# Kernel optimization log

Measured on AMD Instinct MI355X. Metric: run time of the kernel, lower is better.

The kernel has to match this reference:

```python
import jax, jax.numpy as jnp
import numpy as np

TEMP = 0.05
EPS = 1e-8  # matches torch F.cosine_similarity eps default


def setup_inputs() -> dict:
    key = jax.random.key(0)
    k1, k2 = jax.random.split(key)
    B, L, H = 2048, 13, 768
    cls = jax.random.normal(k1, (B, H), dtype=jnp.float32)
    hidden = jax.random.normal(k2, (B, L, H), dtype=jnp.float32)
    return {"cls": cls, "hidden": hidden}


def _normalize(x, axis=-1):
    n = jnp.sqrt(jnp.sum(x * x, axis=axis, keepdims=True))
    return x / jnp.maximum(n, EPS)


def reference(cls, hidden):
    B, L, H = hidden.shape
    cn = _normalize(cls)            # [B, H]
    hn = _normalize(hidden)         # [B, L, H]

    # exp(cos(cls_i, hidden_{i,k}) / temp) -- aligned (diagonal) similarities
    sim_ci_hik = jnp.exp(jnp.einsum('id,ild->il', cn, hn) / TEMP)  # [B, L]

    # exp(cos(cls_i, hidden_{m,n}) / temp) -- all pairs, flattened (m,n)-major
    sim_ci_hmn = jnp.exp(jnp.einsum('id,mnd->imn', cn, hn) / TEMP)  # [B, B, L]
    sim_flat = sim_ci_hmn.reshape(B, B * L)                         # [B, B*L]

    # faithful to original: mask tiles (1 - eye(B)) L times along columns,
    # i.e. zeroes columns c with c % B == i (layout quirk of the source code)
    hmn_mask = jnp.tile(1.0 - jnp.eye(B, dtype=sim_flat.dtype), (1, L))  # [B, B*L]
    s = jnp.sum(sim_flat * hmn_mask, axis=1)                             # [B]

    loss = jnp.mean(-jnp.log(sim_ci_hik) + jnp.log(sim_ci_hik + s[:, None]))
    return loss
```

## Files before the change

### kernel.cpp

```cpp
#include <hip/hip_runtime.h>
#include <cstdint>
#include <cstddef>

#define B_    2048
#define L_    13
#define H_    768
#define NROW  (B_ * L_)
#define RTEMP 20.0f
#define NT    12
#define RS    768
#define NTILE 3328

typedef float f32x4 __attribute__((ext_vector_type(4)));
typedef long  i64x2 __attribute__((ext_vector_type(2)));

static __device__ __forceinline__ unsigned int f2e4m3(float f) {
  unsigned int u = __float_as_uint(f);
  unsigned int s = (u >> 24) & 0x80u;
  unsigned int ua = u & 0x7fffffffu;
  if (ua >= 0x43e80000u) return s | 0x7eu;
  if (ua < 0x3c800000u) {
    int m = (int)rintf(__uint_as_float(ua) * 512.0f);
    return s | (unsigned int)m;
  }
  unsigned int lsb = (ua >> 20) & 1u;
  unsigned int r = ua + 0x7ffffu + lsb;
  int Ee = (int)((r >> 23) & 0xffu) - 127;
  unsigned int mant = (r >> 20) & 7u;
  return s | (unsigned int)(((Ee + 7) << 3) | mant);
}

__device__ __forceinline__ void llds16(const void* g, void* l) {
  __builtin_amdgcn_global_load_lds(
      (const __attribute__((address_space(1))) void*)g,
      (__attribute__((address_space(3))) void*)l, 16, 0, 0);
}

#define BAR do { asm volatile("" ::: "memory");            \
    __builtin_amdgcn_s_barrier();                          \
    asm volatile("" ::: "memory"); } while (0)

#define OFF8(k) ((((k) >> 6) << 6) + (((((k) & 31) >> 3)) << 4) + ((((k) & 32) ? 8 : 0)) + ((k) & 7))

__global__ __launch_bounds__(256) void k_normalize(
    const float* __restrict__ cls, const float* __restrict__ hidden,
    unsigned char* __restrict__ cn8, unsigned char* __restrict__ hn8)
{
  const int wid = threadIdx.x >> 6, lane = threadIdx.x & 63;
  const int row = blockIdx.x * 4 + wid;
  const float4* src; unsigned char* dst;
  if (row < B_) { src = (const float4*)(cls + (size_t)row * H_);           dst = cn8 + (size_t)row * RS; }
  else          { src = (const float4*)(hidden + (size_t)(row - B_) * H_); dst = hn8 + (size_t)(row - B_) * RS; }

  float4 x0 = src[lane], x1 = src[lane + 64], x2 = src[lane + 128];
  float ss = x0.x*x0.x + x0.y*x0.y + x0.z*x0.z + x0.w*x0.w
           + x1.x*x1.x + x1.y*x1.y + x1.z*x1.z + x1.w*x1.w
           + x2.x*x2.x + x2.y*x2.y + x2.z*x2.z + x2.w*x2.w;
#pragma unroll
  for (int m = 1; m < 64; m <<= 1) ss += __shfl_xor(ss, m);
  const float sc = 1.0f / fmaxf(sqrtf(ss), 1e-8f);

  const int k = lane * 4;
  unsigned int p0 = f2e4m3(x0.x*sc) | (f2e4m3(x0.y*sc) << 8) | (f2e4m3(x0.z*sc) << 16) | (f2e4m3(x0.w*sc) << 24);
  unsigned int p1 = f2e4m3(x1.x*sc) | (f2e4m3(x1.y*sc) << 8) | (f2e4m3(x1.z*sc) << 16) | (f2e4m3(x1.w*sc) << 24);
  unsigned int p2 = f2e4m3(x2.x*sc) | (f2e4m3(x2.y*sc) << 8) | (f2e4m3(x2.z*sc) << 16) | (f2e4m3(x2.w*sc) << 24);
  *(unsigned int*)(dst + OFF8(k))       = p0;
  *(unsigned int*)(dst + OFF8(k + 256)) = p1;
  *(unsigned int*)(dst + OFF8(k + 512)) = p2;
}

__global__ __launch_bounds__(256, 4) void k_gemm(
    const unsigned char* __restrict__ cn8,
    const unsigned char* __restrict__ hn8,
    float* __restrict__ S_all,
    float* __restrict__ alignedD)
{
  __shared__ __align__(16) char lds[32768];

  const int tid  = threadIdx.x;
  const int lane = tid & 63;
  const int wid  = tid >> 6;
  const int wm   = wid >> 1;
  const int wn   = wid & 1;
  const int fr   = lane & 15, q = lane >> 4, fr2 = (lane & 15) >> 1;

  const int swz  = ((q | ((fr & 1) << 2)) ^ (fr2 & 7)) << 4;
  const int offA = wm * 4096 + fr2 * 128 + swz;
  const int offB = 8192 + wn * 4096 + fr2 * 128 + swz;

  const int slot_un = (tid & 7) ^ ((tid >> 3) & 7);
  const int srow = 2 * (tid >> 3) + (slot_un >> 2);
  const int scb  = (slot_un & 3) << 4;
  char* ldst = lds + tid * 16;

  const int tile = blockIdx.x;
  const int xcd  = tile & 7;
  const int idx  = tile >> 3;
  const int brow = (idx & 15) << 7;
  const int bcol = (xcd * 26 + (idx >> 4)) << 7;

  const char* gA = (const char*)cn8 + (size_t)(brow + srow) * RS + scb;
  const char* gB = (const char*)hn8 + (size_t)(bcol + srow) * RS + scb;

#define STAGE(sb, t) do {                                         \
    char* d_ = ldst + (sb);                                       \
    const char* a_ = gA + (t) * 64;                               \
    llds16(a_,           d_);                                     \
    llds16(a_ + 64 * RS, d_ + 4096);                              \
    const char* b_ = gB + (t) * 64;                               \
    llds16(b_,           d_ + 8192);                              \
    llds16(b_ + 64 * RS, d_ + 12288);                             \
  } while (0)

  STAGE(0, 0);
  asm volatile("s_waitcnt vmcnt(0)" ::: "memory");
  BAR;

  f32x4 acc[4][4] = {};

  for (int t = 0; t < NT; ++t) {
    if (t + 1 < NT) STAGE(((t + 1) & 1) * 16384, t + 1);

    const char* bb = lds + (t & 1) * 16384;
    i64x2 av[4], bv[4];
#pragma unroll
    for (int i = 0; i < 4; ++i) av[i] = *(const i64x2*)(bb + offA + i * 1024);
#pragma unroll
    for (int i = 0; i < 4; ++i) bv[i] = *(const i64x2*)(bb + offB + i * 1024);

    __builtin_amdgcn_s_setprio(1);
#pragma unroll
    for (int mi = 0; mi < 4; ++mi)
#pragma unroll
      for (int ni = 0; ni < 4; ++ni)
        acc[mi][ni] = __builtin_amdgcn_mfma_f32_16x16x32_fp8_fp8(
            av[mi][0], bv[ni][0], acc[mi][ni], 0, 0, 0);
#pragma unroll
    for (int mi = 0; mi < 4; ++mi)
#pragma unroll
      for (int ni = 0; ni < 4; ++ni)
        acc[mi][ni] = __builtin_amdgcn_mfma_f32_16x16x32_fp8_fp8(
            av[mi][1], bv[ni][1], acc[mi][ni], 0, 0, 0);
    __builtin_amdgcn_s_setprio(0);

    if (t + 1 < NT) {
      asm volatile("s_waitcnt vmcnt(0)" ::: "memory");
      BAR;
    }
  }
#undef STAGE

  const int rowb = brow + wm * 64;
  const int colb = bcol + wn * 64;
#pragma unroll
  for (int mi = 0; mi < 4; ++mi) {
#pragma unroll
    for (int j = 0; j < 4; ++j) {
      const int grow = rowb + mi * 16 + q * 4 + j;
      float v = 0.f;
#pragma unroll
      for (int ni = 0; ni < 4; ++ni) {
        const int gcol = colb + ni * 16 + fr;
        const float a = acc[mi][ni][j];
        if ((unsigned)(gcol - grow * 13) < 13u) alignedD[gcol] = a;
        v += ((gcol & 2047) == grow) ? 0.f : __expf(RTEMP * a);
      }
      v += __shfl_xor(v, 1); v += __shfl_xor(v, 2);
      v += __shfl_xor(v, 4); v += __shfl_xor(v, 8);
      if (fr == 0) atomicAdd(&S_all[grow], v);
    }
  }
}

__global__ __launch_bounds__(256) void k_finalize(
    const float* __restrict__ S_all, const float* __restrict__ alignedD,
    float* __restrict__ out)
{
  const int i = blockIdx.x * 256 + threadIdx.x;
  const int lane = threadIdx.x & 63, wid = threadIdx.x >> 6;
  const float s = S_all[i];
  float accv = 0.f;
#pragma unroll
  for (int l = 0; l < L_; l++) {
    const float d = RTEMP * alignedD[i * L_ + l];
    accv += logf(__expf(d) + s) - d;
  }
#pragma unroll
  for (int m = 1; m < 64; m <<= 1) accv += __shfl_xor(accv, m);
  __shared__ float wsum[4];
  if (lane == 0) wsum[wid] = accv;
  __syncthreads();
  if (threadIdx.x == 0)
    atomicAdd(out, (wsum[0] + wsum[1] + wsum[2] + wsum[3]) * (1.0f / (float)(B_ * L_)));
}

extern "C" void kernel_launch(void* const* d_in, const int* in_sizes, int n_in,
                              void* d_out, int out_size, void* d_ws, size_t ws_size,
                              hipStream_t stream) {
  const float* cls    = (const float*)d_in[0];
  const float* hidden = (const float*)d_in[1];
  float* out = (float*)d_out;

  char* ws = (char*)d_ws;
  unsigned char* hn8 = (unsigned char*)ws;
  unsigned char* cn8 = (unsigned char*)(ws + (size_t)NROW * RS);
  float* S_all    = (float*)(ws + (size_t)NROW * RS + (size_t)B_ * RS);
  float* alignedD = (float*)(ws + (size_t)NROW * RS + (size_t)B_ * RS + B_ * sizeof(float));

  hipMemsetAsync(S_all, 0, B_ * sizeof(float), stream);
  hipMemsetAsync(out, 0, sizeof(float), stream);

  k_normalize<<<(B_ + NROW) / 4, 256, 0, stream>>>(cls, hidden, cn8, hn8);
  k_gemm<<<NTILE, 256, 0, stream>>>(cn8, hn8, S_all, alignedD);
  k_finalize<<<B_ / 256, 256, 0, stream>>>(S_all, alignedD, out);
}
```

Baseline: 101.0 us.

## Give each wave private LDS staging buffers and remove workgroup barriers in GEMM

Each of the four waves now loads its own copy of the A and B sub-tiles it needs into a private 16KB LDS region, double-buffered, and waits only with a per-wave vmcnt counter. This removes the workgroup-wide s_barrier from the main loop. In exchange, LDS use doubles to 64KB and occupancy is lowered to 2 blocks per CU. Global and LDS load traffic also doubles, because each A and B sub-tile is now fetched by two waves. There is a possible hazard: the buffer being refilled may still be read by in-flight LDS reads from the previous iteration, since there is no lgkmcnt wait.

```diff
diff --git a/kernel.cpp b/kernel.cpp
--- a/kernel.cpp
+++ b/kernel.cpp
@@ -35,10 +35,6 @@
       (const __attribute__((address_space(1))) void*)g,
       (__attribute__((address_space(3))) void*)l, 16, 0, 0);
 }
-
-#define BAR do { asm volatile("" ::: "memory");            \
-    __builtin_amdgcn_s_barrier();                          \
-    asm volatile("" ::: "memory"); } while (0)
 
 #define OFF8(k) ((((k) >> 6) << 6) + (((((k) & 31) >> 3)) << 4) + ((((k) & 32) ? 8 : 0)) + ((k) & 7))
 
@@ -69,13 +65,13 @@
   *(unsigned int*)(dst + OFF8(k + 512)) = p2;
 }
 
-__global__ __launch_bounds__(256, 4) void k_gemm(
+__global__ __launch_bounds__(256, 2) void k_gemm(
     const unsigned char* __restrict__ cn8,
     const unsigned char* __restrict__ hn8,
     float* __restrict__ S_all,
     float* __restrict__ alignedD)
 {
-  __shared__ __align__(16) char lds[32768];
+  __shared__ __align__(16) char lds[65536];
 
   const int tid  = threadIdx.x;
   const int lane = tid & 63;
@@ -84,44 +80,52 @@
   const int wn   = wid & 1;
   const int fr   = lane & 15, q = lane >> 4, fr2 = (lane & 15) >> 1;
 
-  const int swz  = ((q | ((fr & 1) << 2)) ^ (fr2 & 7)) << 4;
-  const int offA = wm * 4096 + fr2 * 128 + swz;
-  const int offB = 8192 + wn * 4096 + fr2 * 128 + swz;
-
-  const int slot_un = (tid & 7) ^ ((tid >> 3) & 7);
-  const int srow = 2 * (tid >> 3) + (slot_un >> 2);
-  const int scb  = (slot_un & 3) << 4;
-  char* ldst = lds + tid * 16;
-
   const int tile = blockIdx.x;
   const int xcd  = tile & 7;
   const int idx  = tile >> 3;
   const int brow = (idx & 15) << 7;
   const int bcol = (xcd * 26 + (idx >> 4)) << 7;
 
-  const char* gA = (const char*)cn8 + (size_t)(brow + srow) * RS + scb;
-  const char* gB = (const char*)hn8 + (size_t)(bcol + srow) * RS + scb;
-
-#define STAGE(sb, t) do {                                         \
-    char* d_ = ldst + (sb);                                       \
-    const char* a_ = gA + (t) * 64;                               \
-    llds16(a_,           d_);                                     \
-    llds16(a_ + 64 * RS, d_ + 4096);                              \
-    const char* b_ = gB + (t) * 64;                               \
-    llds16(b_,           d_ + 8192);                              \
-    llds16(b_ + 64 * RS, d_ + 12288);                             \
+  const int line    = lane >> 3;
+  const int slot_un = (lane & 7) ^ (line & 7);
+  const int srw     = 2 * line + (slot_un >> 2);
+  const int scb     = (slot_un & 3) << 4;
+  const char* gAw = (const char*)cn8 + (size_t)(brow + wm * 64 + srw) * RS + scb;
+  const char* gBw = (const char*)hn8 + (size_t)(bcol + wn * 64 + srw) * RS + scb;
+  char* lw = lds + wid * 16384 + lane * 16;
+
+#define STAGE(s, t) do {                                          \
+    char* d_ = lw + (s) * 8192;                                   \
+    const char* a_ = gAw + (t) * 64;                              \
+    llds16(a_,            d_);                                    \
+    llds16(a_ + 16 * RS,  d_ + 1024);                             \
+    llds16(a_ + 32 * RS,  d_ + 2048);                             \
+    llds16(a_ + 48 * RS,  d_ + 3072);                             \
+    const char* b_ = gBw + (t) * 64;                              \
+    llds16(b_,            d_ + 4096);                             \
+    llds16(b_ + 16 * RS,  d_ + 5120);                             \
+    llds16(b_ + 32 * RS,  d_ + 6144);                             \
+    llds16(b_ + 48 * RS,  d_ + 7168);                             \
   } while (0)
 
+  const int swz  = ((q | ((fr & 1) << 2)) ^ (fr2 & 7)) << 4;
+  const int offA = fr2 * 128 + swz;
+  const int offB = 4096 + fr2 * 128 + swz;
+  const char* wbase = lds + wid * 16384;
+
+  f32x4 acc[4][4] = {};
+
   STAGE(0, 0);
-  asm volatile("s_waitcnt vmcnt(0)" ::: "memory");
-  BAR;
-
-  f32x4 acc[4][4] = {};
 
   for (int t = 0; t < NT; ++t) {
-    if (t + 1 < NT) STAGE(((t + 1) & 1) * 16384, t + 1);
-
-    const char* bb = lds + (t & 1) * 16384;
+    if (t + 1 < NT) {
+      STAGE((t + 1) & 1, t + 1);
+      asm volatile("s_waitcnt vmcnt(8)" ::: "memory");
+    } else {
+      asm volatile("s_waitcnt vmcnt(0)" ::: "memory");
+    }
+
+    const char* bb = wbase + (t & 1) * 8192;
     i64x2 av[4], bv[4];
 #pragma unroll
     for (int i = 0; i < 4; ++i) av[i] = *(const i64x2*)(bb + offA + i * 1024);
@@ -142,11 +146,6 @@
         acc[mi][ni] = __builtin_amdgcn_mfma_f32_16x16x32_fp8_fp8(
             av[mi][1], bv[ni][1], acc[mi][ni], 0, 0, 0);
     __builtin_amdgcn_s_setprio(0);
-
-    if (t + 1 < NT) {
-      asm volatile("s_waitcnt vmcnt(0)" ::: "memory");
-      BAR;
-    }
   }
 #undef STAGE
 
```

New measurement: 123.1 us. 1.22x slower.

## Triple-buffer B tiles in GEMM and fold memsets into normalize kernel

Applied to the files above, without the earlier changes.

The GEMM pipeline now keeps A in two LDS buffers and B in three, prefetching B two K-steps ahead and waiting only for the older loads (vmcnt(2)) before each barrier. Loads for the next stage are issued after the current fragments are read from LDS. Global-memory latency should then be hidden better behind the MFMA work. The two hipMemsetAsync calls are removed and block 0 of the normalize kernel zeroes S_all and the output instead, saving two launches. LDS per block grows from 32 KB to 40 KB, which may reduce how many blocks fit on a CU.

```diff
diff --git a/kernel.cpp b/kernel.cpp
--- a/kernel.cpp
+++ b/kernel.cpp
@@ -44,8 +44,15 @@
 
 __global__ __launch_bounds__(256) void k_normalize(
     const float* __restrict__ cls, const float* __restrict__ hidden,
-    unsigned char* __restrict__ cn8, unsigned char* __restrict__ hn8)
+    unsigned char* __restrict__ cn8, unsigned char* __restrict__ hn8,
+    float* __restrict__ S_all, float* __restrict__ out)
 {
+  if (blockIdx.x == 0) {
+#pragma unroll
+    for (int i = 0; i < 8; ++i) S_all[threadIdx.x * 8 + i] = 0.0f;
+    if (threadIdx.x == 0) *out = 0.0f;
+  }
+
   const int wid = threadIdx.x >> 6, lane = threadIdx.x & 63;
   const int row = blockIdx.x * 4 + wid;
   const float4* src; unsigned char* dst;
@@ -75,7 +82,7 @@
     float* __restrict__ S_all,
     float* __restrict__ alignedD)
 {
-  __shared__ __align__(16) char lds[32768];
+  __shared__ __align__(16) char lds[40960];
 
   const int tid  = threadIdx.x;
   const int lane = tid & 63;
@@ -86,7 +93,7 @@
 
   const int swz  = ((q | ((fr & 1) << 2)) ^ (fr2 & 7)) << 4;
   const int offA = wm * 4096 + fr2 * 128 + swz;
-  const int offB = 8192 + wn * 4096 + fr2 * 128 + swz;
+  const int offB = wn * 4096 + fr2 * 128 + swz;
 
   const int slot_un = (tid & 7) ^ ((tid >> 3) & 7);
   const int srow = 2 * (tid >> 3) + (slot_un >> 2);
@@ -102,31 +109,39 @@
   const char* gA = (const char*)cn8 + (size_t)(brow + srow) * RS + scb;
   const char* gB = (const char*)hn8 + (size_t)(bcol + srow) * RS + scb;
 
-#define STAGE(sb, t) do {                                         \
+#define STAGE_A(sb, t) do {                                       \
     char* d_ = ldst + (sb);                                       \
     const char* a_ = gA + (t) * 64;                               \
     llds16(a_,           d_);                                     \
     llds16(a_ + 64 * RS, d_ + 4096);                              \
+  } while (0)
+#define STAGE_B(sb, t) do {                                       \
+    char* d_ = ldst + (sb);                                       \
     const char* b_ = gB + (t) * 64;                               \
-    llds16(b_,           d_ + 8192);                              \
-    llds16(b_ + 64 * RS, d_ + 12288);                             \
+    llds16(b_,           d_);                                     \
+    llds16(b_ + 64 * RS, d_ + 4096);                              \
   } while (0)
 
-  STAGE(0, 0);
-  asm volatile("s_waitcnt vmcnt(0)" ::: "memory");
+  STAGE_A(0, 0);
+  STAGE_B(16384, 0);
+  STAGE_B(16384 + 8192, 1);
+  asm volatile("s_waitcnt vmcnt(2)" ::: "memory");
   BAR;
 
   f32x4 acc[4][4] = {};
 
   for (int t = 0; t < NT; ++t) {
-    if (t + 1 < NT) STAGE(((t + 1) & 1) * 16384, t + 1);
-
-    const char* bb = lds + (t & 1) * 16384;
+    const char* bA = lds + (t & 1) * 8192;
+    const char* bB = lds + 16384 + (t % 3) * 8192;
+
     i64x2 av[4], bv[4];
 #pragma unroll
-    for (int i = 0; i < 4; ++i) av[i] = *(const i64x2*)(bb + offA + i * 1024);
-#pragma unroll
-    for (int i = 0; i < 4; ++i) bv[i] = *(const i64x2*)(bb + offB + i * 1024);
+    for (int i = 0; i < 4; ++i) av[i] = *(const i64x2*)(bA + offA + i * 1024);
+#pragma unroll
+    for (int i = 0; i < 4; ++i) bv[i] = *(const i64x2*)(bB + offB + i * 1024);
+
+    if (t + 1 < NT) STAGE_A(((t + 1) & 1) * 8192, t + 1);
+    if (t + 2 < NT) STAGE_B(16384 + ((t + 2) % 3) * 8192, t + 2);
 
     __builtin_amdgcn_s_setprio(1);
 #pragma unroll
@@ -143,12 +158,11 @@
             av[mi][1], bv[ni][1], acc[mi][ni], 0, 0, 0);
     __builtin_amdgcn_s_setprio(0);
 
-    if (t + 1 < NT) {
-      asm volatile("s_waitcnt vmcnt(0)" ::: "memory");
-      BAR;
-    }
-  }
-#undef STAGE
+    if (t + 2 < NT)      { asm volatile("s_waitcnt vmcnt(2)" ::: "memory"); BAR; }
+    else if (t + 1 < NT) { asm volatile("s_waitcnt vmcnt(0)" ::: "memory"); BAR; }
+  }
+#undef STAGE_A
+#undef STAGE_B
 
   const int rowb = brow + wm * 64;
   const int colb = bcol + wn * 64;
@@ -207,10 +221,7 @@
   float* S_all    = (float*)(ws + (size_t)NROW * RS + (size_t)B_ * RS);
   float* alignedD = (float*)(ws + (size_t)NROW * RS + (size_t)B_ * RS + B_ * sizeof(float));
 
-  hipMemsetAsync(S_all, 0, B_ * sizeof(float), stream);
-  hipMemsetAsync(out, 0, sizeof(float), stream);
-
-  k_normalize<<<(B_ + NROW) / 4, 256, 0, stream>>>(cls, hidden, cn8, hn8);
+  k_normalize<<<(B_ + NROW) / 4, 256, 0, stream>>>(cls, hidden, cn8, hn8, S_all, out);
   k_gemm<<<NTILE, 256, 0, stream>>>(cn8, hn8, S_all, alignedD);
   k_finalize<<<B_ / 256, 256, 0, stream>>>(S_all, alignedD, out);
 }
```

After: 92.15 us (median of 2 runs). 8.7% less time.
